# Kernel optimization log

Measured on AMD Instinct MI355X. Metric: run time of the kernel, lower is better.

## Reference

```python
import jax, jax.numpy as jnp
import numpy as np

D_MODEL = 1024
N_HEADS = 16
HEAD_DIM = D_MODEL // N_HEADS
LENGTHS = np.array([1536, 1024, 1400, 900, 1200, 1300, 1500, 1000])
OFFSETS = np.concatenate([[0], np.cumsum(LENGTHS)]).astype(np.int32)
N_TOT = int(OFFSETS[-1])
LN_EPS = 1e-5


def _pad_meta(offsets):
    # Static (numpy) gather indices: ragged concat [N,D] -> padded [B,Lmax,D]
    offsets = np.asarray(offsets)
    lengths = np.diff(offsets)
    lmax = int(lengths.max())
    tok = np.arange(lmax)[None, :]                      # [1, Lmax]
    valid = tok < lengths[:, None]                      # [B, Lmax] bool
    src = np.where(valid, offsets[:-1, None] + tok, 0)  # [B, Lmax] int
    return src, valid


def setup_inputs() -> dict:
    key = jax.random.key(0)
    ks = jax.random.split(key, 4)
    s = 1.0 / np.sqrt(D_MODEL)
    return {
        "x": jax.random.normal(ks[0], (N_TOT, D_MODEL), jnp.float32),
        "batch_offsets": jnp.asarray(OFFSETS, jnp.int32),
        "in_proj_w": jax.random.normal(ks[1], (3 * D_MODEL, D_MODEL), jnp.float32) * s,
        "in_proj_b": jnp.zeros((3 * D_MODEL,), jnp.float32),
        "out_w": jax.random.normal(ks[2], (D_MODEL, D_MODEL), jnp.float32) * s,
        "out_b": jnp.zeros((D_MODEL,), jnp.float32),
        "ln_g": jnp.ones((D_MODEL,), jnp.float32),
        "ln_b": jnp.zeros((D_MODEL,), jnp.float32),
    }


def reference(x, batch_offsets, in_proj_w, in_proj_b, out_w, out_b, ln_g, ln_b):
    src, valid = _pad_meta(np.asarray(batch_offsets))
    B, L = valid.shape
    vmask = jnp.asarray(valid)
    # deconcat_add_batch_dim: pad to [B, L, D]
    xp = x[src] * vmask[..., None]
    # pre-LayerNorm
    mu = jnp.mean(xp, axis=-1, keepdims=True)
    var = jnp.mean((xp - mu) ** 2, axis=-1, keepdims=True)
    h = (xp - mu) * jax.lax.rsqrt(var + LN_EPS) * ln_g + ln_b
    # fused qkv projection (torch MHA in_proj)
    qkv = h @ in_proj_w.T + in_proj_b                   # [B, L, 3D]
    q, k, v = jnp.split(qkv, 3, axis=-1)
    def heads(t):
        return t.reshape(B, L, N_HEADS, HEAD_DIM).transpose(0, 2, 1, 3)
    q, k, v = heads(q), heads(k), heads(v)              # [B, H, L, hd]
    scores = jnp.einsum("bhqd,bhkd->bhqk", q, k) / np.sqrt(HEAD_DIM)
    scores = jnp.where(vmask[:, None, None, :], scores, -jnp.inf)
    attn = jax.nn.softmax(scores, axis=-1)
    o = jnp.einsum("bhqk,bhkd->bhqd", attn, v)          # [B, H, L, hd]
    o = o.transpose(0, 2, 1, 3).reshape(B, L, D_MODEL)
    o = o @ out_w.T + out_b
    y = xp + o                                          # residual (dropout p=0)
    # remove_batch_dim_and_concat: unpad back to [N, D]
    return y[vmask]
```

## Files before the change

### kernel.cpp

```cpp
#include <hip/hip_runtime.h>
#include <hip/hip_bf16.h>
#include <stdint.h>

#define D_MODEL 1024
#define QKV_LD  3072
#define N_TOT   9860
#define M_PAD   9984
#define LN_EPS  1e-5f

typedef __bf16 bf16_t;
typedef __bf16 bf16x8 __attribute__((ext_vector_type(8)));
typedef float  f32x4  __attribute__((ext_vector_type(4)));
typedef float  f32x16 __attribute__((ext_vector_type(16)));
typedef uint32_t u32x4 __attribute__((ext_vector_type(4)));

__device__ inline unsigned short f2bf(float f) {
  __bf16 h = (__bf16)f;
  return __builtin_bit_cast(unsigned short, h);
}
__device__ inline int imin(int a, int b) { return a < b ? a : b; }

__device__ inline void plswap(uint32_t& a, uint32_t& b) {
  asm("v_permlane32_swap_b32 %0, %1" : "+v"(a), "+v"(b));
}

__device__ inline void gload_lds16(const bf16_t* g, void* l) {
  __builtin_amdgcn_global_load_lds(
      (const __attribute__((address_space(1))) unsigned int*)g,
      (__attribute__((address_space(3))) unsigned int*)l, 16, 0, 0);
}

__global__ __launch_bounds__(256) void cvt_weights(const float* __restrict__ w_in,
                                                   const float* __restrict__ w_out,
                                                   bf16_t* __restrict__ win,
                                                   bf16_t* __restrict__ wout) {
  const int n_in = QKV_LD * D_MODEL / 4;
  int i = blockIdx.x * 256 + threadIdx.x;
  const float* src;
  ushort4* dst;
  int j;
  if (i < n_in) { src = w_in; dst = (ushort4*)win; j = i; }
  else          { src = w_out; dst = (ushort4*)wout; j = i - n_in; }
  float4 v = ((const float4*)src)[j];
  dst[j] = make_ushort4(f2bf(v.x), f2bf(v.y), f2bf(v.z), f2bf(v.w));
}

__global__ __launch_bounds__(256) void ln_kernel(const float* __restrict__ x,
                                                 const float* __restrict__ g,
                                                 const float* __restrict__ b,
                                                 bf16_t* __restrict__ hout) {
  int row = blockIdx.x;
  int t = threadIdx.x;
  if (row >= N_TOT) {
    ((ushort4*)(hout + (size_t)row * D_MODEL))[t] = make_ushort4(0, 0, 0, 0);
    return;
  }
  float4 v = ((const float4*)(x + (size_t)row * D_MODEL))[t];
  float s  = v.x + v.y + v.z + v.w;
  float sq = v.x * v.x + v.y * v.y + v.z * v.z + v.w * v.w;
  #pragma unroll
  for (int off = 1; off < 64; off <<= 1) {
    s  += __shfl_xor(s, off);
    sq += __shfl_xor(sq, off);
  }
  __shared__ float ss[4], ssq[4];
  int wid = t >> 6;
  if ((t & 63) == 0) { ss[wid] = s; ssq[wid] = sq; }
  __syncthreads();
  s  = ss[0] + ss[1] + ss[2] + ss[3];
  sq = ssq[0] + ssq[1] + ssq[2] + ssq[3];
  float mu  = s * (1.0f / 1024.0f);
  float var = sq * (1.0f / 1024.0f) - mu * mu;
  float rs  = rsqrtf(var + LN_EPS);
  float4 gv = ((const float4*)g)[t];
  float4 bv = ((const float4*)b)[t];
  ushort4 o;
  o.x = f2bf((v.x - mu) * rs * gv.x + bv.x);
  o.y = f2bf((v.y - mu) * rs * gv.y + bv.y);
  o.z = f2bf((v.z - mu) * rs * gv.z + bv.z);
  o.w = f2bf((v.w - mu) * rs * gv.w + bv.w);
  ((ushort4*)(hout + (size_t)row * D_MODEL))[t] = o;
}

template<int NCOLS, bool FINAL>
__global__ __launch_bounds__(256) void gemm_bt(const bf16_t* __restrict__ A,
                                               const bf16_t* __restrict__ B,
                                               const float* __restrict__ bias,
                                               bf16_t* __restrict__ Cbf,
                                               float* __restrict__ Cf,
                                               const float* __restrict__ resid) {
  constexpr int K = 1024;
  constexpr int GX = M_PAD / 128;
  constexpr int NWG = GX * (NCOLS / 128);
  int bid = blockIdx.x;
  bid = (bid & 7) * (NWG / 8) + (bid >> 3);
  const int tileM = bid % GX;
  const int tileN = bid / GX;
  const int t = threadIdx.x;
  const int lane = t & 63, wid = t >> 6;
  const int wr = wid >> 1, wc = wid & 1;

  __shared__ bf16_t Asm[128 * 64];
  __shared__ bf16_t Bsm[128 * 64];

  f32x4 acc[4][4];
  #pragma unroll
  for (int m = 0; m < 4; ++m)
    #pragma unroll
    for (int n = 0; n < 4; ++n)
      acc[m][n] = f32x4{0.f, 0.f, 0.f, 0.f};

  const int rowA0 = tileM * 128, rowB0 = tileN * 128;
  const int lrow = lane >> 3;
  const int lch  = lane & 7;

  for (int kt = 0; kt < K / 64; ++kt) {
    __syncthreads();
    const int k0 = kt * 64;
    #pragma unroll
    for (int i = 0; i < 4; ++i) {
      const int r  = wid * 32 + i * 8 + lrow;
      const int sc = lch ^ (r & 7);
      gload_lds16(A + (size_t)(rowA0 + r) * K + k0 + sc * 8,
                  (char*)Asm + (wid * 32 + i * 8) * 128);
      gload_lds16(B + (size_t)(rowB0 + r) * K + k0 + sc * 8,
                  (char*)Bsm + (wid * 32 + i * 8) * 128);
    }
    __syncthreads();
    #pragma unroll
    for (int ks = 0; ks < 2; ++ks) {
      bf16x8 af[4], bfr[4];
      #pragma unroll
      for (int m = 0; m < 4; ++m) {
        int r = wr * 64 + m * 16 + (lane & 15);
        int c = ks * 4 + (lane >> 4);
        af[m] = *(const bf16x8*)((const char*)Asm + r * 128 + ((c ^ (r & 7)) * 16));
      }
      #pragma unroll
      for (int n = 0; n < 4; ++n) {
        int r = wc * 64 + n * 16 + (lane & 15);
        int c = ks * 4 + (lane >> 4);
        bfr[n] = *(const bf16x8*)((const char*)Bsm + r * 128 + ((c ^ (r & 7)) * 16));
      }
      #pragma unroll
      for (int m = 0; m < 4; ++m)
        #pragma unroll
        for (int n = 0; n < 4; ++n)
          acc[m][n] = __builtin_amdgcn_mfma_f32_16x16x32_bf16(af[m], bfr[n], acc[m][n], 0, 0, 0);
    }
  }

  #pragma unroll
  for (int m = 0; m < 4; ++m) {
    int rb = tileM * 128 + wr * 64 + m * 16 + ((lane >> 4) << 2);
    #pragma unroll
    for (int n = 0; n < 4; ++n) {
      int cb = tileN * 128 + wc * 64 + n * 16 + (lane & 15);
      float bv = bias[cb];
      #pragma unroll
      for (int j = 0; j < 4; ++j) {
        int grow = rb + j;
        float val = acc[m][n][j] + bv;
        if constexpr (FINAL) {
          if (grow < N_TOT) {
            size_t idx = (size_t)grow * NCOLS + cb;
            Cf[idx] = resid[idx] + val;
          }
        } else {
          Cbf[(size_t)grow * NCOLS + cb] = (bf16_t)val;
        }
      }
    }
  }
}

__global__ __launch_bounds__(256) void transpose_v(const bf16_t* __restrict__ qkv,
                                                   bf16_t* __restrict__ vt) {
  __shared__ bf16_t tile[64][72];
  const int t = threadIdx.x;
  const int n0 = blockIdx.x * 64, c0 = blockIdx.y * 64;
  #pragma unroll
  for (int it = 0; it < 2; ++it) {
    int idx = it * 256 + t;
    int row = idx >> 3, ch = idx & 7;
    bf16x8 v = *(const bf16x8*)(qkv + (size_t)(n0 + row) * QKV_LD + 2048 + c0 + ch * 8);
    *(bf16x8*)(&tile[row][ch * 8]) = v;
  }
  __syncthreads();
  #pragma unroll
  for (int it = 0; it < 2; ++it) {
    int idx = it * 256 + t;
    int crow = idx >> 3, ng = idx & 7;
    bf16x8 o;
    #pragma unroll
    for (int i = 0; i < 8; ++i) o[i] = tile[ng * 8 + i][crow];
    *(bf16x8*)(vt + (size_t)(c0 + crow) * M_PAD + n0 + ng * 8) = o;
  }
}

__global__ __launch_bounds__(256) void attn_mfma(const bf16_t* __restrict__ qkv,
                                                 const bf16_t* __restrict__ vt,
                                                 bf16_t* __restrict__ obuf) {
  static const int off0_[8] = {0, 7360, 2560, 6060, 4860, 1536, 8860, 3960};
  static const int len_[8]  = {1536, 1500, 1400, 1300, 1200, 1024, 1000, 900};
  static const int ts_[9]   = {0, 12, 24, 35, 46, 56, 64, 72, 80};
  const int tt = blockIdx.x;
  const int h  = blockIdx.y;
  int b = 0;
  #pragma unroll
  for (int i = 1; i < 8; ++i) b += (tt >= ts_[i]);
  const int L     = len_[b];
  const int kbase = off0_[b];
  const int q0    = (tt - ts_[b]) * 128;
  const int tok0  = kbase + q0;
  const int nq    = imin(L - q0, 128);

  const int t = threadIdx.x;
  const int lane = t & 63, w = t >> 6;
  const int qcol = lane & 31, hi = lane >> 5;

  __shared__ char Ks[8192];
  __shared__ char Vs[8192];

  bf16x8 qf[4];
  {
    const bf16_t* qp = qkv + (size_t)(tok0 + w * 32 + qcol) * QKV_LD + h * 64;
    #pragma unroll
    for (int c = 0; c < 4; ++c) {
      bf16x8 v = *(const bf16x8*)(qp + c * 16 + hi * 8);
      #pragma unroll
      for (int i = 0; i < 8; ++i) v[i] = (__bf16)((float)v[i] * 0.125f);
      qf[c] = v;
    }
  }

  f32x16 accO[2];
  #pragma unroll
  for (int db = 0; db < 2; ++db)
    #pragma unroll
    for (int i = 0; i < 16; ++i) accO[db][i] = 0.f;
  float m_r  = -INFINITY;
  float lsum = 0.f;

  const int srow0 = t >> 3, sch = t & 7;

  int4 kreg[2];
  int2 vreg[2][2];
  auto load_tile = [&](int kv0) {
    #pragma unroll
    for (int it = 0; it < 2; ++it) {
      int row = srow0 + it * 32;
      kreg[it] = *(const int4*)(qkv + (size_t)(kbase + kv0 + row) * QKV_LD + 1024 + h * 64 + sch * 8);
      const bf16_t* vp = vt + (size_t)(h * 64 + row) * M_PAD + kbase + kv0 + sch * 8;
      vreg[it][0] = *(const int2*)vp;
      vreg[it][1] = *(const int2*)(vp + 4);
    }
  };

  load_tile(0);

  for (int kv0 = 0; kv0 < L; kv0 += 64) {
    const int nk = imin(L - kv0, 64);
    __syncthreads();
    #pragma unroll
    for (int it = 0; it < 2; ++it) {
      int row = srow0 + it * 32;
      int sw = ((sch ^ (row & 7)) * 16);
      *(int4*)(Ks + row * 128 + sw) = kreg[it];
      int4 vv;
      vv.x = vreg[it][0].x; vv.y = vreg[it][0].y;
      vv.z = vreg[it][1].x; vv.w = vreg[it][1].y;
      *(int4*)(Vs + row * 128 + sw) = vv;
    }
    __syncthreads();
    if (kv0 + 64 < L) load_tile(kv0 + 64);

    f32x16 accS[2];
    #pragma unroll
    for (int kb = 0; kb < 2; ++kb)
      #pragma unroll
      for (int i = 0; i < 16; ++i) accS[kb][i] = 0.f;
    __builtin_amdgcn_s_setprio(1);
    #pragma unroll
    for (int kb = 0; kb < 2; ++kb) {
      int key = kb * 32 + qcol;
      #pragma unroll
      for (int c = 0; c < 4; ++c) {
        bf16x8 kf = *(const bf16x8*)(Ks + key * 128 + (((2 * c + hi) ^ (key & 7)) * 16));
        accS[kb] = __builtin_amdgcn_mfma_f32_32x32x16_bf16(kf, qf[c], accS[kb], 0, 0, 0);
      }
    }
    __builtin_amdgcn_s_setprio(0);

    if (nk < 64) {
      #pragma unroll
      for (int kb = 0; kb < 2; ++kb)
        #pragma unroll
        for (int r = 0; r < 16; ++r)
          if (kb * 32 + (r & 3) + 8 * (r >> 2) + 4 * hi >= nk) accS[kb][r] = -INFINITY;
    }

    float mx = accS[0][0];
    #pragma unroll
    for (int r = 1; r < 16; ++r) mx = fmaxf(mx, accS[0][r]);
    #pragma unroll
    for (int r = 0; r < 16; ++r) mx = fmaxf(mx, accS[1][r]);
    mx = fmaxf(mx, __shfl_xor(mx, 32));

    if (!__all(mx <= m_r + 8.0f)) {
      float mnew = fmaxf(m_r, mx);
      float scl  = __expf(m_r - mnew);
      lsum *= scl;
      #pragma unroll
      for (int db = 0; db < 2; ++db)
        #pragma unroll
        for (int i = 0; i < 16; ++i) accO[db][i] *= scl;
      m_r = mnew;
    }

    bf16x8 pb[2][2];
    #pragma unroll
    for (int kb = 0; kb < 2; ++kb) {
      uint32_t G[4][2];
      #pragma unroll
      for (int j = 0; j < 4; ++j) {
        float p0 = __expf(accS[kb][4 * j + 0] - m_r);
        float p1 = __expf(accS[kb][4 * j + 1] - m_r);
        float p2 = __expf(accS[kb][4 * j + 2] - m_r);
        float p3 = __expf(accS[kb][4 * j + 3] - m_r);
        lsum += (p0 + p1) + (p2 + p3);
        G[j][0] = (uint32_t)f2bf(p0) | ((uint32_t)f2bf(p1) << 16);
        G[j][1] = (uint32_t)f2bf(p2) | ((uint32_t)f2bf(p3) << 16);
      }
      #pragma unroll
      for (int c = 0; c < 2; ++c) {
        uint32_t ax = G[2 * c][0], bx = G[2 * c + 1][0];
        uint32_t ay = G[2 * c][1], by = G[2 * c + 1][1];
        plswap(ax, bx);
        plswap(ay, by);
        u32x4 u; u[0] = ax; u[1] = ay; u[2] = bx; u[3] = by;
        pb[kb][c] = __builtin_bit_cast(bf16x8, u);
      }
    }

    __builtin_amdgcn_s_setprio(1);
    #pragma unroll
    for (int kb = 0; kb < 2; ++kb)
      #pragma unroll
      for (int c = 0; c < 2; ++c) {
        int ch = 4 * kb + 2 * c + hi;
        #pragma unroll
        for (int db = 0; db < 2; ++db) {
          int dim = db * 32 + qcol;
          bf16x8 vf = *(const bf16x8*)(Vs + dim * 128 + ((ch ^ (dim & 7)) * 16));
          accO[db] = __builtin_amdgcn_mfma_f32_32x32x16_bf16(vf, pb[kb][c], accO[db], 0, 0, 0);
        }
      }
    __builtin_amdgcn_s_setprio(0);
  }

  float l = lsum + __shfl_xor(lsum, 32);
  const int qlocal = w * 32 + qcol;
  if (qlocal < nq) {
    float inv = 1.f / l;
    bf16_t* op = obuf + (size_t)(tok0 + qlocal) * D_MODEL + h * 64;
    #pragma unroll
    for (int db = 0; db < 2; ++db)
      #pragma unroll
      for (int rr = 0; rr < 4; ++rr) {
        float v0 = accO[db][4 * rr + 0] * inv;
        float v1 = accO[db][4 * rr + 1] * inv;
        float v2 = accO[db][4 * rr + 2] * inv;
        float v3 = accO[db][4 * rr + 3] * inv;
        uint2 u;
        u.x = (uint32_t)f2bf(v0) | ((uint32_t)f2bf(v1) << 16);
        u.y = (uint32_t)f2bf(v2) | ((uint32_t)f2bf(v3) << 16);
        *(uint2*)(op + db * 32 + rr * 8 + hi * 4) = u;
      }
  }
}

extern "C" void kernel_launch(void* const* d_in, const int* in_sizes, int n_in,
                              void* d_out, int out_size, void* d_ws, size_t ws_size,
                              hipStream_t stream) {
  const float* x     = (const float*)d_in[0];
  const float* w_in  = (const float*)d_in[2];
  const float* b_in  = (const float*)d_in[3];
  const float* w_out = (const float*)d_in[4];
  const float* b_out = (const float*)d_in[5];
  const float* ln_g  = (const float*)d_in[6];
  const float* ln_b  = (const float*)d_in[7];
  float* out = (float*)d_out;

  char* ws = (char*)d_ws;
  const size_t SZ_H   = (size_t)M_PAD * D_MODEL * 2;
  const size_t SZ_QKV = (size_t)M_PAD * QKV_LD * 2;
  const size_t SZ_O   = SZ_H;
  const size_t SZ_WIN = (size_t)QKV_LD * D_MODEL * 2;
  const size_t SZ_WO  = (size_t)D_MODEL * D_MODEL * 2;
  if (ws_size < SZ_H + SZ_QKV + SZ_O + SZ_WIN + SZ_WO) return;

  bf16_t* h_bf    = (bf16_t*)ws;
  bf16_t* qkv_bf  = (bf16_t*)(ws + SZ_H);
  bf16_t* o_bf    = (bf16_t*)(ws + SZ_H + SZ_QKV);
  bf16_t* win_bf  = (bf16_t*)(ws + SZ_H + SZ_QKV + SZ_O);
  bf16_t* wout_bf = (bf16_t*)(ws + SZ_H + SZ_QKV + SZ_O + SZ_WIN);

  cvt_weights<<<(QKV_LD * D_MODEL / 4 + D_MODEL * D_MODEL / 4) / 256, 256, 0, stream>>>(
      w_in, w_out, win_bf, wout_bf);

  ln_kernel<<<M_PAD, 256, 0, stream>>>(x, ln_g, ln_b, h_bf);

  gemm_bt<QKV_LD, false><<<(M_PAD / 128) * (QKV_LD / 128), 256, 0, stream>>>(
      h_bf, win_bf, b_in, qkv_bf, nullptr, nullptr);

  bf16_t* vt = h_bf;
  transpose_v<<<dim3(M_PAD / 64, D_MODEL / 64), 256, 0, stream>>>(qkv_bf, vt);

  attn_mfma<<<dim3(80, 16), 256, 0, stream>>>(qkv_bf, vt, o_bf);

  gemm_bt<D_MODEL, true><<<(M_PAD / 128) * (D_MODEL / 128), 256, 0, stream>>>(
      o_bf, wout_bf, b_out, nullptr, out, x);
}
```

Baseline: 335.5 us.

## Add 256x256 double-buffered QKV GEMM and halve attention query tile

Adds a new 512-thread GEMM kernel with 256x256 output tiles and double-buffered direct-to-LDS loads, used for the QKV projection in place of the 128x128 kernel. It aims to raise arithmetic intensity and overlap global loads with MFMA work. Separately, attention blocks now process 64 queries with 128 threads instead of 128 with 256, doubling the grid to 157x16 for better CU occupancy on ragged lengths. In exchange each block reloads K/V tiles more often and the large GEMM uses 128KB of LDS, which limits it to one block per CU.

```diff
diff --git a/kernel.cpp b/kernel.cpp
--- a/kernel.cpp
+++ b/kernel.cpp
@@ -82,6 +82,119 @@
   ((ushort4*)(hout + (size_t)row * D_MODEL))[t] = o;
 }
 
+template<int NCOLS>
+__global__ __launch_bounds__(512) void gemm256(const bf16_t* __restrict__ A,
+                                               const bf16_t* __restrict__ B,
+                                               const float* __restrict__ bias,
+                                               bf16_t* __restrict__ Cbf) {
+  constexpr int K = 1024, NKT = K / 64;
+  constexpr int GX = M_PAD / 256;
+  constexpr int NWG = GX * (NCOLS / 256);
+  int bid = blockIdx.x;
+  {
+    constexpr int q = NWG / 8, r = NWG % 8;
+    int x = bid & 7, o = bid >> 3;
+    bid = (x < r ? x * (q + 1) : r * (q + 1) + (x - r) * q) + o;
+  }
+  const int tileM = bid % GX;
+  const int tileN = bid / GX;
+  const int t = threadIdx.x;
+  const int lane = t & 63, wid = t >> 6;
+  const int wr = wid >> 2, wc = wid & 3;
+
+  __shared__ bf16_t As[2][256 * 64];
+  __shared__ bf16_t Bs[2][256 * 64];
+
+  f32x4 acc[8][4];
+  #pragma unroll
+  for (int m = 0; m < 8; ++m)
+    #pragma unroll
+    for (int n = 0; n < 4; ++n)
+      acc[m][n] = f32x4{0.f, 0.f, 0.f, 0.f};
+
+  const int rowA0 = tileM * 256, rowB0 = tileN * 256;
+  const int lrow = lane >> 3;
+  const int lch  = lane & 7;
+
+  auto stage = [&](int buf, int kt) {
+    const int k0 = kt * 64;
+    #pragma unroll
+    for (int i = 0; i < 4; ++i) {
+      const int r  = wid * 32 + i * 8 + lrow;
+      const int sc = lch ^ (r & 7);
+      gload_lds16(A + (size_t)(rowA0 + r) * K + k0 + sc * 8,
+                  (char*)&As[buf][(wid * 32 + i * 8) * 64]);
+      gload_lds16(B + (size_t)(rowB0 + r) * K + k0 + sc * 8,
+                  (char*)&Bs[buf][(wid * 32 + i * 8) * 64]);
+    }
+  };
+
+  stage(0, 0);
+
+  for (int kt = 0; kt < NKT; ++kt) {
+    const int cur = kt & 1;
+    if (kt + 1 < NKT) {
+      stage(cur ^ 1, kt + 1);
+      asm volatile("s_waitcnt vmcnt(8)" ::: "memory");
+    } else {
+      asm volatile("s_waitcnt vmcnt(0)" ::: "memory");
+    }
+    __builtin_amdgcn_s_barrier();
+    __builtin_amdgcn_sched_barrier(0);
+
+    const char* Ab = (const char*)&As[cur][0];
+    const char* Bb = (const char*)&Bs[cur][0];
+
+    bf16x8 bfr[4][2];
+    #pragma unroll
+    for (int n = 0; n < 4; ++n)
+      #pragma unroll
+      for (int ks = 0; ks < 2; ++ks) {
+        int r = wc * 64 + n * 16 + (lane & 15);
+        int c = ks * 4 + (lane >> 4);
+        bfr[n][ks] = *(const bf16x8*)(Bb + r * 128 + ((c ^ (r & 7)) * 16));
+      }
+    #pragma unroll
+    for (int p = 0; p < 4; ++p) {
+      bf16x8 af[2][2];
+      #pragma unroll
+      for (int mm = 0; mm < 2; ++mm)
+        #pragma unroll
+        for (int ks = 0; ks < 2; ++ks) {
+          int r = wr * 128 + (p * 2 + mm) * 16 + (lane & 15);
+          int c = ks * 4 + (lane >> 4);
+          af[mm][ks] = *(const bf16x8*)(Ab + r * 128 + ((c ^ (r & 7)) * 16));
+        }
+      __builtin_amdgcn_s_setprio(1);
+      #pragma unroll
+      for (int mm = 0; mm < 2; ++mm)
+        #pragma unroll
+        for (int n = 0; n < 4; ++n)
+          #pragma unroll
+          for (int ks = 0; ks < 2; ++ks)
+            acc[p * 2 + mm][n] =
+                __builtin_amdgcn_mfma_f32_16x16x32_bf16(af[mm][ks], bfr[n][ks],
+                                                        acc[p * 2 + mm][n], 0, 0, 0);
+      __builtin_amdgcn_s_setprio(0);
+    }
+    __builtin_amdgcn_sched_barrier(0);
+    __builtin_amdgcn_s_barrier();
+  }
+
+  #pragma unroll
+  for (int m = 0; m < 8; ++m) {
+    int rb = tileM * 256 + wr * 128 + m * 16 + ((lane >> 4) << 2);
+    #pragma unroll
+    for (int n = 0; n < 4; ++n) {
+      int cb = tileN * 256 + wc * 64 + n * 16 + (lane & 15);
+      float bv = bias[cb];
+      #pragma unroll
+      for (int j = 0; j < 4; ++j)
+        Cbf[(size_t)(rb + j) * NCOLS + cb] = (bf16_t)(acc[m][n][j] + bv);
+    }
+  }
+}
+
 template<int NCOLS, bool FINAL>
 __global__ __launch_bounds__(256) void gemm_bt(const bf16_t* __restrict__ A,
                                                const bf16_t* __restrict__ B,
@@ -198,12 +311,12 @@
   }
 }
 
-__global__ __launch_bounds__(256) void attn_mfma(const bf16_t* __restrict__ qkv,
+__global__ __launch_bounds__(128) void attn_mfma(const bf16_t* __restrict__ qkv,
                                                  const bf16_t* __restrict__ vt,
                                                  bf16_t* __restrict__ obuf) {
   static const int off0_[8] = {0, 7360, 2560, 6060, 4860, 1536, 8860, 3960};
   static const int len_[8]  = {1536, 1500, 1400, 1300, 1200, 1024, 1000, 900};
-  static const int ts_[9]   = {0, 12, 24, 35, 46, 56, 64, 72, 80};
+  static const int ts_[9]   = {0, 24, 48, 70, 91, 110, 126, 142, 157};
   const int tt = blockIdx.x;
   const int h  = blockIdx.y;
   int b = 0;
@@ -211,9 +324,9 @@
   for (int i = 1; i < 8; ++i) b += (tt >= ts_[i]);
   const int L     = len_[b];
   const int kbase = off0_[b];
-  const int q0    = (tt - ts_[b]) * 128;
+  const int q0    = (tt - ts_[b]) * 64;
   const int tok0  = kbase + q0;
-  const int nq    = imin(L - q0, 128);
+  const int nq    = imin(L - q0, 64);
 
   const int t = threadIdx.x;
   const int lane = t & 63, w = t >> 6;
@@ -244,12 +357,12 @@
 
   const int srow0 = t >> 3, sch = t & 7;
 
-  int4 kreg[2];
-  int2 vreg[2][2];
+  int4 kreg[4];
+  int2 vreg[4][2];
   auto load_tile = [&](int kv0) {
     #pragma unroll
-    for (int it = 0; it < 2; ++it) {
-      int row = srow0 + it * 32;
+    for (int it = 0; it < 4; ++it) {
+      int row = srow0 + it * 16;
       kreg[it] = *(const int4*)(qkv + (size_t)(kbase + kv0 + row) * QKV_LD + 1024 + h * 64 + sch * 8);
       const bf16_t* vp = vt + (size_t)(h * 64 + row) * M_PAD + kbase + kv0 + sch * 8;
       vreg[it][0] = *(const int2*)vp;
@@ -263,8 +376,8 @@
     const int nk = imin(L - kv0, 64);
     __syncthreads();
     #pragma unroll
-    for (int it = 0; it < 2; ++it) {
-      int row = srow0 + it * 32;
+    for (int it = 0; it < 4; ++it) {
+      int row = srow0 + it * 16;
       int sw = ((sch ^ (row & 7)) * 16);
       *(int4*)(Ks + row * 128 + sw) = kreg[it];
       int4 vv;
@@ -411,13 +524,13 @@
 
   ln_kernel<<<M_PAD, 256, 0, stream>>>(x, ln_g, ln_b, h_bf);
 
-  gemm_bt<QKV_LD, false><<<(M_PAD / 128) * (QKV_LD / 128), 256, 0, stream>>>(
-      h_bf, win_bf, b_in, qkv_bf, nullptr, nullptr);
+  gemm256<QKV_LD><<<(M_PAD / 256) * (QKV_LD / 256), 512, 0, stream>>>(
+      h_bf, win_bf, b_in, qkv_bf);
 
   bf16_t* vt = h_bf;
   transpose_v<<<dim3(M_PAD / 64, D_MODEL / 64), 256, 0, stream>>>(qkv_bf, vt);
 
-  attn_mfma<<<dim3(80, 16), 256, 0, stream>>>(qkv_bf, vt, o_bf);
+  attn_mfma<<<dim3(157, 16), 128, 0, stream>>>(qkv_bf, vt, o_bf);
 
   gemm_bt<D_MODEL, true><<<(M_PAD / 128) * (D_MODEL / 128), 256, 0, stream>>>(
       o_bf, wout_bf, b_out, nullptr, out, x);
```

Measured after the change: 340.5 us. About the same (+1.5%).
